# Kernel tuning notes

Hardware: AMD Instinct MI355X
Metric: run time of the kernel (lower is better)

Reference implementation:

```python
import jax, jax.numpy as jnp
import numpy as np

N = 50000        # nodes
E = 800000       # directed edges (before self-loops)
F_IN = 128       # input node features
HID = 32         # hidden channels per head
HEADS = 4
NCLS = 8
EPS_BN = 1e-5
NEG_SLOPE = 0.2  # GATConv LeakyReLU default


def setup_inputs() -> dict:
    key = jax.random.key(0)
    ks = jax.random.split(key, 16)
    rn = lambda k, shape, s=0.1: jax.random.normal(k, shape, jnp.float32) * s
    inp = {}
    inp["x"] = jax.random.normal(ks[0], (N, F_IN), jnp.float32)
    inp["edge_index"] = jax.random.randint(ks[1], (2, E), 0, N, dtype=jnp.int32)
    # layer 0: F_IN -> HEADS*HID (concat)
    inp["W0"] = rn(ks[2], (F_IN, HEADS * HID))
    inp["as0"] = rn(ks[3], (HEADS, HID))
    inp["ad0"] = rn(ks[4], (HEADS, HID))
    inp["b0"] = jnp.zeros((HEADS * HID,), jnp.float32)
    inp["g0"] = jnp.ones((HEADS * HID,), jnp.float32)
    inp["bb0"] = jnp.zeros((HEADS * HID,), jnp.float32)
    inp["rm0"] = jnp.zeros((HEADS * HID,), jnp.float32)
    inp["rv0"] = jnp.ones((HEADS * HID,), jnp.float32)
    # layer 1: HEADS*HID -> HEADS*HID (concat)
    inp["W1"] = rn(ks[5], (HEADS * HID, HEADS * HID))
    inp["as1"] = rn(ks[6], (HEADS, HID))
    inp["ad1"] = rn(ks[7], (HEADS, HID))
    inp["b1"] = jnp.zeros((HEADS * HID,), jnp.float32)
    inp["g1"] = jnp.ones((HEADS * HID,), jnp.float32)
    inp["bb1"] = jnp.zeros((HEADS * HID,), jnp.float32)
    inp["rm1"] = jnp.zeros((HEADS * HID,), jnp.float32)
    inp["rv1"] = jnp.ones((HEADS * HID,), jnp.float32)
    # layer 2: HEADS*HID -> NCLS, heads=1, concat=False
    inp["W2"] = rn(ks[8], (HEADS * HID, NCLS))
    inp["as2"] = rn(ks[9], (1, NCLS))
    inp["ad2"] = rn(ks[10], (1, NCLS))
    inp["b2"] = jnp.zeros((NCLS,), jnp.float32)
    return inp


def gat_conv(x, src, dst, W, att_s, att_d, bias, H, C, concat):
    """PyG-style GATConv (eval mode, self-loops already appended to src/dst)."""
    n = x.shape[0]
    h = (x @ W).reshape(n, H, C)                       # [N,H,C]
    a_s = (h * att_s).sum(-1)                          # [N,H]
    a_d = (h * att_d).sum(-1)                          # [N,H]
    e = jax.nn.leaky_relu(a_s[src] + a_d[dst], NEG_SLOPE)  # [E,H]
    # numerically-stable segment softmax over incoming edges of each dst node
    m = jax.ops.segment_max(e, dst, num_segments=n)
    m = jnp.where(jnp.isfinite(m), m, 0.0)
    ex = jnp.exp(e - m[dst])
    den = jax.ops.segment_sum(ex, dst, num_segments=n)
    alpha = ex / (den[dst] + 1e-16)                    # [E,H]
    out = jax.ops.segment_sum(h[src] * alpha[:, :, None], dst, num_segments=n)  # [N,H,C]
    out = out.reshape(n, H * C) if concat else out.mean(axis=1)
    return out + bias


def bn_eval(x, g, b, rm, rv):
    return (x - rm) * jax.lax.rsqrt(rv + EPS_BN) * g + b


def reference(x, edge_index, W0, as0, ad0, b0, g0, bb0, rm0, rv0,
              W1, as1, ad1, b1, g1, bb1, rm1, rv1, W2, as2, ad2, b2):
    n = x.shape[0]
    loop = jnp.arange(n, dtype=edge_index.dtype)       # self-loops (PyG default)
    src = jnp.concatenate([edge_index[0], loop])
    dst = jnp.concatenate([edge_index[1], loop])
    h = gat_conv(x, src, dst, W0, as0, ad0, b0, HEADS, HID, True)
    h = jax.nn.elu(bn_eval(h, g0, bb0, rm0, rv0))
    h = gat_conv(h, src, dst, W1, as1, ad1, b1, HEADS, HID, True)
    h = jax.nn.elu(bn_eval(h, g1, bb1, rm1, rv1))
    h = gat_conv(h, src, dst, W2, as2, ad2, b2, 1, NCLS, False)
    return jax.nn.log_softmax(h, axis=1)
```

## Files before the change

### kernel.cpp

```cpp
#include <hip/hip_runtime.h>
#include <math.h>

#define N_NODES 50000
#define N_EDGES 800000
#define ET (N_EDGES + N_NODES)
#define FDIM 128
#define HEADS 4
#define HID 32
#define NCLS 8
#define NEG 0.2f
#define EPS_BN 1e-5f

#define BSH 8
#define NBUCK ((N_NODES + 255) >> BSH)
#define EPB 4096

typedef __attribute__((ext_vector_type(8))) short short8;
typedef __attribute__((ext_vector_type(4))) float f32x4;

__device__ __forceinline__ float lrelu(float e) { return e > 0.f ? e : NEG * e; }
__device__ __forceinline__ float bflo(unsigned u) { return __uint_as_float(u << 16); }
__device__ __forceinline__ float bfhi(unsigned u) { return __uint_as_float(u & 0xffff0000u); }
__device__ __forceinline__ unsigned f2bf(float f) {
    unsigned b = __float_as_uint(f);
    return (b + 0x7fffu + ((b >> 16) & 1u)) >> 16;
}


__global__ __launch_bounds__(256) void bucket_hist(const int* __restrict__ ei,
                                                   int* __restrict__ bhist) {
    __shared__ unsigned h[NBUCK];
    int tid = threadIdx.x;
    int e0 = blockIdx.x * EPB;
    for (int i = tid; i < NBUCK; i += 256) h[i] = 0;
    __syncthreads();
    #pragma unroll
    for (int k = 0; k < EPB / 256; k++) {
        int e = e0 + k * 256 + tid;
        if (e < ET) {
            int d = (e < N_EDGES) ? ei[N_EDGES + e] : (e - N_EDGES);
            atomicAdd(&h[d >> BSH], 1u);
        }
    }
    __syncthreads();
    for (int i = tid; i < NBUCK; i += 256)
        if (h[i]) atomicAdd(&bhist[i], (int)h[i]);
}

__global__ __launch_bounds__(256) void scan_buckets(const int* __restrict__ bhist,
                                                    int* __restrict__ boffs,
                                                    int* __restrict__ bcur,
                                                    int* __restrict__ offs) {
    __shared__ int s[256];
    int tid = threadIdx.x;
    int v = (tid < NBUCK) ? bhist[tid] : 0;
    s[tid] = v;
    __syncthreads();
    for (int off = 1; off < 256; off <<= 1) {
        int x = (tid >= off) ? s[tid - off] : 0;
        __syncthreads();
        s[tid] += x;
        __syncthreads();
    }
    int excl = s[tid] - v;
    if (tid < NBUCK) { boffs[tid] = excl; bcur[tid] = excl; }
    if (tid == 0) { boffs[NBUCK] = ET; offs[N_NODES] = ET; }
}

__global__ __launch_bounds__(256) void partition_pairs(const int* __restrict__ ei,
                                                       int* __restrict__ bcur,
                                                       int2* __restrict__ pairs) {
    __shared__ unsigned hist[NBUCK];
    __shared__ unsigned base[NBUCK];
    int tid = threadIdx.x;
    int e0 = blockIdx.x * EPB;
    for (int i = tid; i < NBUCK; i += 256) hist[i] = 0;
    __syncthreads();
    #pragma unroll
    for (int k = 0; k < EPB / 256; k++) {
        int e = e0 + k * 256 + tid;
        if (e < ET) {
            int d = (e < N_EDGES) ? ei[N_EDGES + e] : (e - N_EDGES);
            atomicAdd(&hist[d >> BSH], 1u);
        }
    }
    __syncthreads();
    for (int i = tid; i < NBUCK; i += 256) {
        unsigned h = hist[i];
        base[i] = h ? (unsigned)atomicAdd(&bcur[i], (int)h) : 0u;
        hist[i] = 0;
    }
    __syncthreads();
    #pragma unroll
    for (int k = 0; k < EPB / 256; k++) {
        int e = e0 + k * 256 + tid;
        if (e < ET) {
            int s, d;
            if (e < N_EDGES) { s = ei[e]; d = ei[N_EDGES + e]; }
            else             { s = d = e - N_EDGES; }
            int b = d >> BSH;
            unsigned lpos = atomicAdd(&hist[b], 1u);
            pairs[base[b] + lpos] = make_int2(s, d);
        }
    }
}

__global__ __launch_bounds__(256) void group_bucket(const int2* __restrict__ pairs,
                                                    const int* __restrict__ boffs,
                                                    int* __restrict__ offs,
                                                    int* __restrict__ ssrc) {
    __shared__ int cnt[256];
    __shared__ int pfx[256];
    int b = blockIdx.x, tid = threadIdx.x;
    int n0 = b << BSH;
    int base = boffs[b], end = boffs[b + 1];
    cnt[tid] = 0;
    __syncthreads();
    for (int i = base + tid; i < end; i += 256)
        atomicAdd(&cnt[pairs[i].y & 255], 1);
    __syncthreads();
    int v = cnt[tid];
    pfx[tid] = v;
    __syncthreads();
    for (int off = 1; off < 256; off <<= 1) {
        int x = (tid >= off) ? pfx[tid - off] : 0;
        __syncthreads();
        pfx[tid] += x;
        __syncthreads();
    }
    int excl = pfx[tid] - v;
    if (n0 + tid < N_NODES) offs[n0 + tid] = base + excl;
    cnt[tid] = excl;
    __syncthreads();
    for (int i = base + tid; i < end; i += 256) {
        int2 p = pairs[i];
        int pos = atomicAdd(&cnt[p.y & 255], 1);
        ssrc[base + pos] = p.x;
    }
}


#define CAST_B 3125
#define PACK_B 64

__global__ void prep_inputs(const float* __restrict__ x, unsigned short* __restrict__ xb,
                            const float* __restrict__ W0, unsigned short* __restrict__ W0p,
                            const float* __restrict__ W1, unsigned short* __restrict__ W1p) {
    int b = blockIdx.x, tid = threadIdx.x;
    if (b < CAST_B) {
        int i = b * 256 + tid;
        const float4* p = (const float4*)x + (size_t)i * 2;
        float4 a = p[0], c = p[1];
        uint4 o;
        o.x = f2bf(a.x) | (f2bf(a.y) << 16);
        o.y = f2bf(a.z) | (f2bf(a.w) << 16);
        o.z = f2bf(c.x) | (f2bf(c.y) << 16);
        o.w = f2bf(c.z) | (f2bf(c.w) << 16);
        ((uint4*)xb)[i] = o;
    } else {
        int pb = b - CAST_B;
        const float* W = (pb < PACK_B) ? W0 : W1;
        unsigned short* Wp = (pb < PACK_B) ? W0p : W1p;
        int o = (pb & (PACK_B - 1)) * 256 + tid;
        int j = o & 7, lane = (o >> 3) & 63, kc = (o >> 9) & 3, t = o >> 11;
        int k = kc * 32 + ((lane >> 4) << 3) + j;
        int n = t * 16 + (lane & 15);
        Wp[o] = (unsigned short)f2bf(W[k * 128 + n]);
    }
}


__global__ __launch_bounds__(256) void gemm_attn(
        const unsigned short* __restrict__ Ab, const unsigned short* __restrict__ Wp,
        const float* __restrict__ att_s, const float* __restrict__ att_d,
        unsigned short* __restrict__ Hb, float* __restrict__ asn, float* __restrict__ adn,
        int M) {
    __shared__ float tiles[64 * 132];
    int tid = threadIdx.x;
    int wv = tid >> 6, lane = tid & 63;
    int base = blockIdx.x * 64;
    int mrow = base + wv * 16 + (lane & 15);
    if (mrow >= M) mrow = M - 1;
    int koff = (lane >> 4) * 8;

    f32x4 acc[8];
    #pragma unroll
    for (int t = 0; t < 8; t++) acc[t] = (f32x4){0.f, 0.f, 0.f, 0.f};

    #pragma unroll
    for (int kc = 0; kc < 4; kc++) {
        short8 a = *(const short8*)(Ab + (size_t)mrow * 128 + kc * 32 + koff);
        #pragma unroll
        for (int t = 0; t < 8; t++) {
            short8 b = *(const short8*)(Wp + (((t * 4 + kc) * 64 + lane) << 3));
            acc[t] = __builtin_amdgcn_mfma_f32_16x16x32_bf16(a, b, acc[t], 0, 0, 0);
        }
    }

    int rbase = wv * 16 + (lane >> 4) * 4;
    int col = lane & 15;
    #pragma unroll
    for (int t = 0; t < 8; t++)
        #pragma unroll
        for (int r = 0; r < 4; r++)
            tiles[(rbase + r) * 132 + t * 16 + col] = acc[t][r];
    __syncthreads();

    #pragma unroll
    for (int it = 0; it < 4; it++) {
        int u = tid + it * 256;
        int rl = u >> 4, cg = u & 15;
        int row = base + rl;
        if (row < M) {
            const float* p = tiles + rl * 132 + cg * 8;
            float4 v0 = *(const float4*)(p);
            float4 v1 = *(const float4*)(p + 4);
            uint4 o;
            o.x = f2bf(v0.x) | (f2bf(v0.y) << 16);
            o.y = f2bf(v0.z) | (f2bf(v0.w) << 16);
            o.z = f2bf(v1.x) | (f2bf(v1.y) << 16);
            o.w = f2bf(v1.z) | (f2bf(v1.w) << 16);
            *(uint4*)(Hb + (size_t)row * 128 + cg * 8) = o;
        }
    }

    {
        int rl = tid >> 2, hd = tid & 3;
        int row = base + rl;
        if (row < M) {
            const float* hrow = tiles + rl * 132 + hd * 32;
            const float* as = att_s + hd * 32;
            const float* ad = att_d + hd * 32;
            float ps = 0.f, pd = 0.f;
            #pragma unroll
            for (int i = 0; i < 8; i++) {
                float4 hv = *(const float4*)(hrow + i * 4);
                float4 sv = *(const float4*)(as + i * 4);
                float4 dv = *(const float4*)(ad + i * 4);
                ps += hv.x * sv.x + hv.y * sv.y + hv.z * sv.z + hv.w * sv.w;
                pd += hv.x * dv.x + hv.y * dv.y + hv.z * dv.z + hv.w * dv.w;
            }
            asn[row * 4 + hd] = ps;
            adn[row * 4 + hd] = pd;
        }
    }
}


__global__ __launch_bounds__(256) void aggregate(
        const unsigned short* __restrict__ hb, const float* __restrict__ asn,
        const float* __restrict__ adn, const int* __restrict__ offs,
        const int* __restrict__ ssrc, const float* __restrict__ bias,
        const float* __restrict__ gamma, const float* __restrict__ beta,
        const float* __restrict__ rmean, const float* __restrict__ rvar,
        unsigned short* __restrict__ outb) {
    __shared__ int2 sPair[4][4][72];
    int wv = threadIdx.x >> 6;
    int node = blockIdx.x * 4 + wv;
    if (node >= N_NODES) return;
    int lane = threadIdx.x & 63;
    int hd = lane >> 4;
    int beg = offs[node], deg = offs[node + 1] - beg;
    float4 ad4 = *(const float4*)(adn + node * 4);

    if (lane < 32) sPair[wv][lane >> 3][64 + (lane & 7)] = make_int2(0, 0);

    float4 den4 = make_float4(0.f, 0.f, 0.f, 0.f);
    float acc0 = 0.f, acc1 = 0.f;
    const unsigned short* hlane = hb + 2 * lane;
    const int2* pp = &sPair[wv][hd][0];

    auto phaseC = [&](int cnt) {
        int bound = (cnt + 7) & ~7;
        for (int i = 0; i < bound; i += 8) {
            int2 p0 = pp[i],     p1 = pp[i + 1], p2 = pp[i + 2], p3 = pp[i + 3];
            int2 p4 = pp[i + 4], p5 = pp[i + 5], p6 = pp[i + 6], p7 = pp[i + 7];
            unsigned u0 = *(const unsigned*)(hlane + (((unsigned)p0.x) << 7));
            unsigned u1 = *(const unsigned*)(hlane + (((unsigned)p1.x) << 7));
            unsigned u2 = *(const unsigned*)(hlane + (((unsigned)p2.x) << 7));
            unsigned u3 = *(const unsigned*)(hlane + (((unsigned)p3.x) << 7));
            unsigned u4 = *(const unsigned*)(hlane + (((unsigned)p4.x) << 7));
            unsigned u5 = *(const unsigned*)(hlane + (((unsigned)p5.x) << 7));
            unsigned u6 = *(const unsigned*)(hlane + (((unsigned)p6.x) << 7));
            unsigned u7 = *(const unsigned*)(hlane + (((unsigned)p7.x) << 7));
            acc0 += __int_as_float(p0.y) * bflo(u0); acc1 += __int_as_float(p0.y) * bfhi(u0);
            acc0 += __int_as_float(p1.y) * bflo(u1); acc1 += __int_as_float(p1.y) * bfhi(u1);
            acc0 += __int_as_float(p2.y) * bflo(u2); acc1 += __int_as_float(p2.y) * bfhi(u2);
            acc0 += __int_as_float(p3.y) * bflo(u3); acc1 += __int_as_float(p3.y) * bfhi(u3);
            acc0 += __int_as_float(p4.y) * bflo(u4); acc1 += __int_as_float(p4.y) * bfhi(u4);
            acc0 += __int_as_float(p5.y) * bflo(u5); acc1 += __int_as_float(p5.y) * bfhi(u5);
            acc0 += __int_as_float(p6.y) * bflo(u6); acc1 += __int_as_float(p6.y) * bfhi(u6);
            acc0 += __int_as_float(p7.y) * bflo(u7); acc1 += __int_as_float(p7.y) * bfhi(u7);
        }
    };

    for (int base0 = 0; base0 < deg; base0 += 64) {
        int j = base0 + lane;
        int s = 0;
        float4 w4 = make_float4(0.f, 0.f, 0.f, 0.f);
        if (j < deg) {
            s = ssrc[beg + j];
            float4 a = *(const float4*)(asn + s * 4);
            w4.x = __expf(lrelu(a.x + ad4.x));
            w4.y = __expf(lrelu(a.y + ad4.y));
            w4.z = __expf(lrelu(a.z + ad4.z));
            w4.w = __expf(lrelu(a.w + ad4.w));
            den4.x += w4.x; den4.y += w4.y; den4.z += w4.z; den4.w += w4.w;
        }
        sPair[wv][0][lane] = make_int2(s, __float_as_int(w4.x));
        sPair[wv][1][lane] = make_int2(s, __float_as_int(w4.y));
        sPair[wv][2][lane] = make_int2(s, __float_as_int(w4.z));
        sPair[wv][3][lane] = make_int2(s, __float_as_int(w4.w));
        int cnt = deg - base0; if (cnt > 64) cnt = 64;
        phaseC(cnt);
    }

    #pragma unroll
    for (int off = 32; off; off >>= 1) {
        den4.x += __shfl_xor(den4.x, off);
        den4.y += __shfl_xor(den4.y, off);
        den4.z += __shfl_xor(den4.z, off);
        den4.w += __shfl_xor(den4.w, off);
    }
    float den = (hd & 2) ? ((hd & 1) ? den4.w : den4.z)
                         : ((hd & 1) ? den4.y : den4.x);
    float inv = 1.f / (den + 1e-16f);

    int c0 = lane * 2;
    float2 bi = *(const float2*)(bias + c0);
    float2 gm = *(const float2*)(gamma + c0);
    float2 bt = *(const float2*)(beta + c0);
    float2 rm = *(const float2*)(rmean + c0);
    float2 rv = *(const float2*)(rvar + c0);
    float o0 = acc0 * inv + bi.x;
    float o1 = acc1 * inv + bi.y;
    o0 = (o0 - rm.x) * rsqrtf(rv.x + EPS_BN) * gm.x + bt.x;
    o1 = (o1 - rm.y) * rsqrtf(rv.y + EPS_BN) * gm.y + bt.y;
    o0 = (o0 > 0.f) ? o0 : expm1f(o0);
    o1 = (o1 > 0.f) ? o1 : expm1f(o1);
    *(unsigned*)(outb + (size_t)node * 128 + c0) = f2bf(o0) | (f2bf(o1) << 16);
}


__global__ __launch_bounds__(256) void gemm2_fused(
        const unsigned short* __restrict__ xb, const float* __restrict__ W2,
        const float* __restrict__ as2, const float* __restrict__ ad2,
        float* __restrict__ h2, float* __restrict__ asn, float* __restrict__ adn) {
    __shared__ float sW[128 * 8];
    __shared__ float sas[8], sad[8];
    int tid = threadIdx.x;
    for (int i = tid; i < 1024; i += 256) sW[i] = W2[i];
    if (tid < 8) { sas[tid] = as2[tid]; sad[tid] = ad2[tid]; }
    __syncthreads();
    int node = blockIdx.x * 256 + tid;
    if (node >= N_NODES) return;
    const uint4* xr = (const uint4*)(xb + (size_t)node * 128);
    float acc[8];
    #pragma unroll
    for (int c = 0; c < 8; c++) acc[c] = 0.f;
    for (int k8 = 0; k8 < 16; k8++) {
        uint4 u = xr[k8];
        float f[8] = { bflo(u.x), bfhi(u.x), bflo(u.y), bfhi(u.y),
                       bflo(u.z), bfhi(u.z), bflo(u.w), bfhi(u.w) };
        int kb = k8 * 8;
        #pragma unroll
        for (int q = 0; q < 8; q++)
            #pragma unroll
            for (int c = 0; c < 8; c++)
                acc[c] += f[q] * sW[(kb + q) * 8 + c];
    }
    float ps = 0.f, pd = 0.f;
    #pragma unroll
    for (int c = 0; c < 8; c++) {
        h2[(size_t)node * 8 + c] = acc[c];
        ps += acc[c] * sas[c];
        pd += acc[c] * sad[c];
    }
    asn[node] = ps;
    adn[node] = pd;
}


__global__ __launch_bounds__(256) void aggregate2(
        const float* __restrict__ h2, const float* __restrict__ asn,
        const float* __restrict__ adn, const int* __restrict__ offs,
        const int* __restrict__ ssrc, const float* __restrict__ b2,
        float* __restrict__ out) {
    __shared__ int2 sPair[4][64];
    int wv = threadIdx.x >> 6;
    int node = blockIdx.x * 4 + wv;
    if (node >= N_NODES) return;
    int lane = threadIdx.x & 63;
    int g = lane >> 3, c = lane & 7;
    int beg = offs[node], end = offs[node + 1];
    int deg = end - beg;
    float adv = adn[node];

    float den = 0.f, acc = 0.f;
    auto phaseC = [&](int cnt) {
        int nIt = (cnt + 15) >> 4;
        const int2* pp = &sPair[wv][0];
        for (int i = 0; i < nIt; i++) {
            int e = i * 16 + g;
            int2 p0 = pp[e];
            int2 p1 = pp[e + 8];
            acc += __int_as_float(p0.y) * h2[(((unsigned)p0.x) << 3) + c];
            acc += __int_as_float(p1.y) * h2[(((unsigned)p1.x) << 3) + c];
        }
    };

    for (int base = 0; base < deg; base += 64) {
        int j = base + lane;
        int s = 0; float w = 0.f;
        if (j < deg) {
            s = ssrc[beg + j];
            w = __expf(lrelu(asn[s] + adv));
            den += w;
        }
        sPair[wv][lane] = make_int2(s, __float_as_int(w));
        int cnt = deg - base; if (cnt > 64) cnt = 64;
        phaseC(cnt);
    }

    acc += __shfl_xor(acc, 8); acc += __shfl_xor(acc, 16); acc += __shfl_xor(acc, 32);
    #pragma unroll
    for (int off = 32; off; off >>= 1) den += __shfl_xor(den, off);

    float o = acc / (den + 1e-16f) + b2[c];
    float mx = o;
    mx = fmaxf(mx, __shfl_xor(mx, 1));
    mx = fmaxf(mx, __shfl_xor(mx, 2));
    mx = fmaxf(mx, __shfl_xor(mx, 4));
    float ex = __expf(o - mx);
    float sm = ex;
    sm += __shfl_xor(sm, 1); sm += __shfl_xor(sm, 2); sm += __shfl_xor(sm, 4);
    if (g == 0) out[(size_t)node * 8 + c] = o - mx - logf(sm);
}


extern "C" void kernel_launch(void* const* d_in, const int* in_sizes, int n_in,
                              void* d_out, int out_size, void* d_ws, size_t ws_size,
                              hipStream_t stream) {
    const float* x   = (const float*)d_in[0];
    const int*   ei  = (const int*)d_in[1];
    const float* W0  = (const float*)d_in[2];
    const float* as0 = (const float*)d_in[3];
    const float* ad0 = (const float*)d_in[4];
    const float* b0  = (const float*)d_in[5];
    const float* g0  = (const float*)d_in[6];
    const float* bb0 = (const float*)d_in[7];
    const float* rm0 = (const float*)d_in[8];
    const float* rv0 = (const float*)d_in[9];
    const float* W1  = (const float*)d_in[10];
    const float* as1 = (const float*)d_in[11];
    const float* ad1 = (const float*)d_in[12];
    const float* b1  = (const float*)d_in[13];
    const float* g1  = (const float*)d_in[14];
    const float* bb1 = (const float*)d_in[15];
    const float* rm1 = (const float*)d_in[16];
    const float* rv1 = (const float*)d_in[17];
    const float* W2  = (const float*)d_in[18];
    const float* as2 = (const float*)d_in[19];
    const float* ad2 = (const float*)d_in[20];
    const float* b2  = (const float*)d_in[21];
    float* out = (float*)d_out;

    char* w = (char*)d_ws;
    size_t off = 0;
    auto carve = [&](size_t bytes) {
        void* p = w + off;
        off += (bytes + 255) & ~(size_t)255;
        return p;
    };
    unsigned short* xb   = (unsigned short*)carve((size_t)N_NODES * 128 * 2);
    unsigned short* Hb   = (unsigned short*)carve((size_t)N_NODES * 128 * 2);
    unsigned short* Xb   = (unsigned short*)carve((size_t)N_NODES * 128 * 2);
    unsigned short* W0p  = (unsigned short*)carve(16384 * 2);
    unsigned short* W1p  = (unsigned short*)carve(16384 * 2);
    int*   offs   = (int*)carve((size_t)(N_NODES + 1) * 4);
    int*   bhist  = (int*)carve((size_t)NBUCK * 4);
    int*   boffs  = (int*)carve((size_t)(NBUCK + 1) * 4);
    int*   bcur   = (int*)carve((size_t)NBUCK * 4);
    int*   ssrc   = (int*)carve((size_t)ET * 4);
    int2*  pairs  = (int2*)carve((size_t)ET * 8);
    float* asn    = (float*)carve((size_t)N_NODES * 4 * 4);
    float* adn    = (float*)carve((size_t)N_NODES * 4 * 4);
    float* h2     = (float*)carve((size_t)N_NODES * 8 * 4);
    float* as2n   = (float*)carve((size_t)N_NODES * 4);
    float* ad2n   = (float*)carve((size_t)N_NODES * 4);
    (void)ws_size; (void)in_sizes; (void)n_in; (void)out_size;

    const int NB = (N_NODES + 255) / 256;
    const int GB = (N_NODES + 63) / 64;
    const int PB = (ET + EPB - 1) / EPB;

    hipMemsetAsync(bhist, 0, (size_t)NBUCK * 4, stream);
    bucket_hist<<<PB, 256, 0, stream>>>(ei, bhist);
    scan_buckets<<<1, 256, 0, stream>>>(bhist, boffs, bcur, offs);
    partition_pairs<<<PB, 256, 0, stream>>>(ei, bcur, pairs);
    group_bucket<<<NBUCK, 256, 0, stream>>>(pairs, boffs, offs, ssrc);

    prep_inputs<<<CAST_B + 2 * PACK_B, 256, 0, stream>>>(x, xb, W0, W0p, W1, W1p);

    gemm_attn<<<GB, 256, 0, stream>>>(xb, W0p, as0, ad0, Hb, asn, adn, N_NODES);
    aggregate<<<(N_NODES + 3) / 4, 256, 0, stream>>>(Hb, asn, adn, offs, ssrc,
                                                     b0, g0, bb0, rm0, rv0, Xb);
    gemm_attn<<<GB, 256, 0, stream>>>(Xb, W1p, as1, ad1, Hb, asn, adn, N_NODES);
    aggregate<<<(N_NODES + 3) / 4, 256, 0, stream>>>(Hb, asn, adn, offs, ssrc,
                                                     b1, g1, bb1, rm1, rv1, Xb);
    gemm2_fused<<<NB, 256, 0, stream>>>(Xb, W2, as2, ad2, h2, as2n, ad2n);
    aggregate2<<<(N_NODES + 3) / 4, 256, 0, stream>>>(h2, as2n, ad2n, offs, ssrc, b2, out);
}
```

Measured before the change: 289.8 us.

## Merge prep with histogram kernel and widen aggregate gathers to 8-byte loads

```diff
diff --git a/kernel.cpp b/kernel.cpp
--- a/kernel.cpp
+++ b/kernel.cpp
@@ -14,6 +14,7 @@
 #define BSH 8
 #define NBUCK ((N_NODES + 255) >> BSH)
 #define EPB 4096
+#define PB ((ET + EPB - 1) / EPB)
 
 typedef __attribute__((ext_vector_type(8))) short short8;
 typedef __attribute__((ext_vector_type(4))) float f32x4;
@@ -27,24 +28,51 @@
 }
 
 
-__global__ __launch_bounds__(256) void bucket_hist(const int* __restrict__ ei,
-                                                   int* __restrict__ bhist) {
+#define CAST_B 3125
+#define PACK_B 64
+
+__global__ __launch_bounds__(256) void prep_and_hist(
+        const int* __restrict__ ei, int* __restrict__ bhist,
+        const float* __restrict__ x, unsigned short* __restrict__ xb,
+        const float* __restrict__ W0, unsigned short* __restrict__ W0p,
+        const float* __restrict__ W1, unsigned short* __restrict__ W1p) {
     __shared__ unsigned h[NBUCK];
-    int tid = threadIdx.x;
-    int e0 = blockIdx.x * EPB;
-    for (int i = tid; i < NBUCK; i += 256) h[i] = 0;
-    __syncthreads();
-    #pragma unroll
-    for (int k = 0; k < EPB / 256; k++) {
-        int e = e0 + k * 256 + tid;
-        if (e < ET) {
-            int d = (e < N_EDGES) ? ei[N_EDGES + e] : (e - N_EDGES);
-            atomicAdd(&h[d >> BSH], 1u);
-        }
-    }
-    __syncthreads();
-    for (int i = tid; i < NBUCK; i += 256)
-        if (h[i]) atomicAdd(&bhist[i], (int)h[i]);
+    int b = blockIdx.x, tid = threadIdx.x;
+    if (b < PB) {
+        int e0 = b * EPB;
+        for (int i = tid; i < NBUCK; i += 256) h[i] = 0;
+        __syncthreads();
+        #pragma unroll
+        for (int k = 0; k < EPB / 256; k++) {
+            int e = e0 + k * 256 + tid;
+            if (e < ET) {
+                int d = (e < N_EDGES) ? ei[N_EDGES + e] : (e - N_EDGES);
+                atomicAdd(&h[d >> BSH], 1u);
+            }
+        }
+        __syncthreads();
+        for (int i = tid; i < NBUCK; i += 256)
+            if (h[i]) atomicAdd(&bhist[i], (int)h[i]);
+    } else if (b < PB + CAST_B) {
+        int i = (b - PB) * 256 + tid;
+        const float4* p = (const float4*)x + (size_t)i * 2;
+        float4 a = p[0], c = p[1];
+        uint4 o;
+        o.x = f2bf(a.x) | (f2bf(a.y) << 16);
+        o.y = f2bf(a.z) | (f2bf(a.w) << 16);
+        o.z = f2bf(c.x) | (f2bf(c.y) << 16);
+        o.w = f2bf(c.z) | (f2bf(c.w) << 16);
+        ((uint4*)xb)[i] = o;
+    } else {
+        int pb = b - PB - CAST_B;
+        const float* W = (pb < PACK_B) ? W0 : W1;
+        unsigned short* Wp = (pb < PACK_B) ? W0p : W1p;
+        int o = (pb & (PACK_B - 1)) * 256 + tid;
+        int j = o & 7, lane = (o >> 3) & 63, kc = (o >> 9) & 3, t = o >> 11;
+        int k = kc * 32 + ((lane >> 4) << 3) + j;
+        int n = t * 16 + (lane & 15);
+        Wp[o] = (unsigned short)f2bf(W[k * 128 + n]);
+    }
 }
 
 __global__ __launch_bounds__(256) void scan_buckets(const int* __restrict__ bhist,
@@ -136,36 +164,6 @@
         int2 p = pairs[i];
         int pos = atomicAdd(&cnt[p.y & 255], 1);
         ssrc[base + pos] = p.x;
-    }
-}
-
-
-#define CAST_B 3125
-#define PACK_B 64
-
-__global__ void prep_inputs(const float* __restrict__ x, unsigned short* __restrict__ xb,
-                            const float* __restrict__ W0, unsigned short* __restrict__ W0p,
-                            const float* __restrict__ W1, unsigned short* __restrict__ W1p) {
-    int b = blockIdx.x, tid = threadIdx.x;
-    if (b < CAST_B) {
-        int i = b * 256 + tid;
-        const float4* p = (const float4*)x + (size_t)i * 2;
-        float4 a = p[0], c = p[1];
-        uint4 o;
-        o.x = f2bf(a.x) | (f2bf(a.y) << 16);
-        o.y = f2bf(a.z) | (f2bf(a.w) << 16);
-        o.z = f2bf(c.x) | (f2bf(c.y) << 16);
-        o.w = f2bf(c.z) | (f2bf(c.w) << 16);
-        ((uint4*)xb)[i] = o;
-    } else {
-        int pb = b - CAST_B;
-        const float* W = (pb < PACK_B) ? W0 : W1;
-        unsigned short* Wp = (pb < PACK_B) ? W0p : W1p;
-        int o = (pb & (PACK_B - 1)) * 256 + tid;
-        int j = o & 7, lane = (o >> 3) & 63, kc = (o >> 9) & 3, t = o >> 11;
-        int k = kc * 32 + ((lane >> 4) << 3) + j;
-        int n = t * 16 + (lane & 15);
-        Wp[o] = (unsigned short)f2bf(W[k * 128 + n]);
     }
 }
 
@@ -259,62 +257,73 @@
     int node = blockIdx.x * 4 + wv;
     if (node >= N_NODES) return;
     int lane = threadIdx.x & 63;
+    int half = lane >> 5;
+    int cl = lane & 31;
     int hd = lane >> 4;
     int beg = offs[node], deg = offs[node + 1] - beg;
     float4 ad4 = *(const float4*)(adn + node * 4);
 
-    if (lane < 32) sPair[wv][lane >> 3][64 + (lane & 7)] = make_int2(0, 0);
-
     float4 den4 = make_float4(0.f, 0.f, 0.f, 0.f);
-    float acc0 = 0.f, acc1 = 0.f;
-    const unsigned short* hlane = hb + 2 * lane;
-    const int2* pp = &sPair[wv][hd][0];
+    float a0 = 0.f, a1 = 0.f, a2 = 0.f, a3 = 0.f;
+    const char* hbase = (const char*)hb + cl * 8;
+    int hsel = (cl >> 3);
+    const int2* pp = &sPair[wv][hsel][0];
 
     auto phaseC = [&](int cnt) {
-        int bound = (cnt + 7) & ~7;
-        for (int i = 0; i < bound; i += 8) {
-            int2 p0 = pp[i],     p1 = pp[i + 1], p2 = pp[i + 2], p3 = pp[i + 3];
-            int2 p4 = pp[i + 4], p5 = pp[i + 5], p6 = pp[i + 6], p7 = pp[i + 7];
-            unsigned u0 = *(const unsigned*)(hlane + (((unsigned)p0.x) << 7));
-            unsigned u1 = *(const unsigned*)(hlane + (((unsigned)p1.x) << 7));
-            unsigned u2 = *(const unsigned*)(hlane + (((unsigned)p2.x) << 7));
-            unsigned u3 = *(const unsigned*)(hlane + (((unsigned)p3.x) << 7));
-            unsigned u4 = *(const unsigned*)(hlane + (((unsigned)p4.x) << 7));
-            unsigned u5 = *(const unsigned*)(hlane + (((unsigned)p5.x) << 7));
-            unsigned u6 = *(const unsigned*)(hlane + (((unsigned)p6.x) << 7));
-            unsigned u7 = *(const unsigned*)(hlane + (((unsigned)p7.x) << 7));
-            acc0 += __int_as_float(p0.y) * bflo(u0); acc1 += __int_as_float(p0.y) * bfhi(u0);
-            acc0 += __int_as_float(p1.y) * bflo(u1); acc1 += __int_as_float(p1.y) * bfhi(u1);
-            acc0 += __int_as_float(p2.y) * bflo(u2); acc1 += __int_as_float(p2.y) * bfhi(u2);
-            acc0 += __int_as_float(p3.y) * bflo(u3); acc1 += __int_as_float(p3.y) * bfhi(u3);
-            acc0 += __int_as_float(p4.y) * bflo(u4); acc1 += __int_as_float(p4.y) * bfhi(u4);
-            acc0 += __int_as_float(p5.y) * bflo(u5); acc1 += __int_as_float(p5.y) * bfhi(u5);
-            acc0 += __int_as_float(p6.y) * bflo(u6); acc1 += __int_as_float(p6.y) * bfhi(u6);
-            acc0 += __int_as_float(p7.y) * bflo(u7); acc1 += __int_as_float(p7.y) * bfhi(u7);
+        int bound = (cnt + 15) & ~15;
+        for (int i = 0; i < bound; i += 16) {
+            int2 p0 = pp[i + 0 + half],  p1 = pp[i + 2 + half];
+            int2 p2 = pp[i + 4 + half],  p3 = pp[i + 6 + half];
+            int2 p4 = pp[i + 8 + half],  p5 = pp[i + 10 + half];
+            int2 p6 = pp[i + 12 + half], p7 = pp[i + 14 + half];
+            uint2 u0 = *(const uint2*)(hbase + (unsigned)p0.x);
+            uint2 u1 = *(const uint2*)(hbase + (unsigned)p1.x);
+            uint2 u2 = *(const uint2*)(hbase + (unsigned)p2.x);
+            uint2 u3 = *(const uint2*)(hbase + (unsigned)p3.x);
+            uint2 u4 = *(const uint2*)(hbase + (unsigned)p4.x);
+            uint2 u5 = *(const uint2*)(hbase + (unsigned)p5.x);
+            uint2 u6 = *(const uint2*)(hbase + (unsigned)p6.x);
+            uint2 u7 = *(const uint2*)(hbase + (unsigned)p7.x);
+            float w0 = __int_as_float(p0.y), w1 = __int_as_float(p1.y);
+            float w2 = __int_as_float(p2.y), w3 = __int_as_float(p3.y);
+            float w4 = __int_as_float(p4.y), w5 = __int_as_float(p5.y);
+            float w6 = __int_as_float(p6.y), w7 = __int_as_float(p7.y);
+            a0 += w0 * bflo(u0.x); a1 += w0 * bfhi(u0.x); a2 += w0 * bflo(u0.y); a3 += w0 * bfhi(u0.y);
+            a0 += w1 * bflo(u1.x); a1 += w1 * bfhi(u1.x); a2 += w1 * bflo(u1.y); a3 += w1 * bfhi(u1.y);
+            a0 += w2 * bflo(u2.x); a1 += w2 * bfhi(u2.x); a2 += w2 * bflo(u2.y); a3 += w2 * bfhi(u2.y);
+            a0 += w3 * bflo(u3.x); a1 += w3 * bfhi(u3.x); a2 += w3 * bflo(u3.y); a3 += w3 * bfhi(u3.y);
+            a0 += w4 * bflo(u4.x); a1 += w4 * bfhi(u4.x); a2 += w4 * bflo(u4.y); a3 += w4 * bfhi(u4.y);
+            a0 += w5 * bflo(u5.x); a1 += w5 * bfhi(u5.x); a2 += w5 * bflo(u5.y); a3 += w5 * bfhi(u5.y);
+            a0 += w6 * bflo(u6.x); a1 += w6 * bfhi(u6.x); a2 += w6 * bflo(u6.y); a3 += w6 * bfhi(u6.y);
+            a0 += w7 * bflo(u7.x); a1 += w7 * bfhi(u7.x); a2 += w7 * bflo(u7.y); a3 += w7 * bfhi(u7.y);
         }
     };
 
     for (int base0 = 0; base0 < deg; base0 += 64) {
         int j = base0 + lane;
-        int s = 0;
-        float4 w4 = make_float4(0.f, 0.f, 0.f, 0.f);
+        int soff = 0;
+        float4 w4v = make_float4(0.f, 0.f, 0.f, 0.f);
         if (j < deg) {
-            s = ssrc[beg + j];
+            int s = ssrc[beg + j];
+            soff = s << 8;
             float4 a = *(const float4*)(asn + s * 4);
-            w4.x = __expf(lrelu(a.x + ad4.x));
-            w4.y = __expf(lrelu(a.y + ad4.y));
-            w4.z = __expf(lrelu(a.z + ad4.z));
-            w4.w = __expf(lrelu(a.w + ad4.w));
-            den4.x += w4.x; den4.y += w4.y; den4.z += w4.z; den4.w += w4.w;
-        }
-        sPair[wv][0][lane] = make_int2(s, __float_as_int(w4.x));
-        sPair[wv][1][lane] = make_int2(s, __float_as_int(w4.y));
-        sPair[wv][2][lane] = make_int2(s, __float_as_int(w4.z));
-        sPair[wv][3][lane] = make_int2(s, __float_as_int(w4.w));
+            w4v.x = __expf(lrelu(a.x + ad4.x));
+            w4v.y = __expf(lrelu(a.y + ad4.y));
+            w4v.z = __expf(lrelu(a.z + ad4.z));
+            w4v.w = __expf(lrelu(a.w + ad4.w));
+            den4.x += w4v.x; den4.y += w4v.y; den4.z += w4v.z; den4.w += w4v.w;
+        }
+        sPair[wv][0][lane] = make_int2(soff, __float_as_int(w4v.x));
+        sPair[wv][1][lane] = make_int2(soff, __float_as_int(w4v.y));
+        sPair[wv][2][lane] = make_int2(soff, __float_as_int(w4v.z));
+        sPair[wv][3][lane] = make_int2(soff, __float_as_int(w4v.w));
         int cnt = deg - base0; if (cnt > 64) cnt = 64;
         phaseC(cnt);
     }
-
+    (void)hd;
+
+    a0 += __shfl_xor(a0, 32); a1 += __shfl_xor(a1, 32);
+    a2 += __shfl_xor(a2, 32); a3 += __shfl_xor(a3, 32);
     #pragma unroll
     for (int off = 32; off; off >>= 1) {
         den4.x += __shfl_xor(den4.x, off);
@@ -322,23 +331,31 @@
         den4.z += __shfl_xor(den4.z, off);
         den4.w += __shfl_xor(den4.w, off);
     }
-    float den = (hd & 2) ? ((hd & 1) ? den4.w : den4.z)
-                         : ((hd & 1) ? den4.y : den4.x);
-    float inv = 1.f / (den + 1e-16f);
-
-    int c0 = lane * 2;
-    float2 bi = *(const float2*)(bias + c0);
-    float2 gm = *(const float2*)(gamma + c0);
-    float2 bt = *(const float2*)(beta + c0);
-    float2 rm = *(const float2*)(rmean + c0);
-    float2 rv = *(const float2*)(rvar + c0);
-    float o0 = acc0 * inv + bi.x;
-    float o1 = acc1 * inv + bi.y;
-    o0 = (o0 - rm.x) * rsqrtf(rv.x + EPS_BN) * gm.x + bt.x;
-    o1 = (o1 - rm.y) * rsqrtf(rv.y + EPS_BN) * gm.y + bt.y;
-    o0 = (o0 > 0.f) ? o0 : expm1f(o0);
-    o1 = (o1 > 0.f) ? o1 : expm1f(o1);
-    *(unsigned*)(outb + (size_t)node * 128 + c0) = f2bf(o0) | (f2bf(o1) << 16);
+    if (half == 0) {
+        float den = (hsel & 2) ? ((hsel & 1) ? den4.w : den4.z)
+                               : ((hsel & 1) ? den4.y : den4.x);
+        float inv = 1.f / (den + 1e-16f);
+        int c0 = cl * 4;
+        float4 bi = *(const float4*)(bias + c0);
+        float4 gm = *(const float4*)(gamma + c0);
+        float4 bt = *(const float4*)(beta + c0);
+        float4 rm = *(const float4*)(rmean + c0);
+        float4 rv = *(const float4*)(rvar + c0);
+        float o0 = a0 * inv + bi.x, o1 = a1 * inv + bi.y;
+        float o2 = a2 * inv + bi.z, o3 = a3 * inv + bi.w;
+        o0 = (o0 - rm.x) * rsqrtf(rv.x + EPS_BN) * gm.x + bt.x;
+        o1 = (o1 - rm.y) * rsqrtf(rv.y + EPS_BN) * gm.y + bt.y;
+        o2 = (o2 - rm.z) * rsqrtf(rv.z + EPS_BN) * gm.z + bt.z;
+        o3 = (o3 - rm.w) * rsqrtf(rv.w + EPS_BN) * gm.w + bt.w;
+        o0 = (o0 > 0.f) ? o0 : expm1f(o0);
+        o1 = (o1 > 0.f) ? o1 : expm1f(o1);
+        o2 = (o2 > 0.f) ? o2 : expm1f(o2);
+        o3 = (o3 > 0.f) ? o3 : expm1f(o3);
+        uint2 ob;
+        ob.x = f2bf(o0) | (f2bf(o1) << 16);
+        ob.y = f2bf(o2) | (f2bf(o3) << 16);
+        *(uint2*)(outb + (size_t)node * 128 + c0) = ob;
+    }
 }
 
 
@@ -492,15 +509,13 @@
 
     const int NB = (N_NODES + 255) / 256;
     const int GB = (N_NODES + 63) / 64;
-    const int PB = (ET + EPB - 1) / EPB;
 
     hipMemsetAsync(bhist, 0, (size_t)NBUCK * 4, stream);
-    bucket_hist<<<PB, 256, 0, stream>>>(ei, bhist);
+    prep_and_hist<<<PB + CAST_B + 2 * PACK_B, 256, 0, stream>>>(ei, bhist, x, xb,
+                                                                W0, W0p, W1, W1p);
     scan_buckets<<<1, 256, 0, stream>>>(bhist, boffs, bcur, offs);
     partition_pairs<<<PB, 256, 0, stream>>>(ei, bcur, pairs);
     group_bucket<<<NBUCK, 256, 0, stream>>>(pairs, boffs, offs, ssrc);
-
-    prep_inputs<<<CAST_B + 2 * PACK_B, 256, 0, stream>>>(x, xb, W0, W0p, W1, W1p);
 
     gemm_attn<<<GB, 256, 0, stream>>>(xb, W0p, as0, ad0, Hb, asn, adn, N_NODES);
     aggregate<<<(N_NODES + 3) / 4, 256, 0, stream>>>(Hb, asn, adn, offs, ssrc,
```

Result: slower. 295.6 us (+2.0%).
